# Optimization experiments

Measured on AMD Instinct MI355X. Metric: run time of the kernel, lower is better.

The kernel has to match this reference:

```python
import jax, jax.numpy as jnp
import numpy as np

NUM_HEADS = 6


def dwconv_tokens(tokens, H, W, w, b, stride):
    # tokens: (B, N, C) -> depthwise conv in (B, C, H, W) -> (B, N', C)
    B, N, C = tokens.shape
    x = tokens.transpose(0, 2, 1).reshape(B, C, H, W)
    y = jax.lax.conv_general_dilated(
        x, w, window_strides=(stride, stride), padding=[(1, 1), (1, 1)],
        feature_group_count=C, dimension_numbers=('NCHW', 'OIHW', 'NCHW'))
    y = y + b[None, :, None, None]
    Bc, Cc, Hs, Ws = y.shape
    return y.reshape(Bc, Cc, Hs * Ws).transpose(0, 2, 1), Hs, Ws


def neg_softmax(a):
    # sign(x) * softmax(|x|) along last axis
    return jnp.sign(a) * jax.nn.softmax(jnp.abs(a), axis=-1)


def split_heads(t, nh):
    B, N, C = t.shape
    return t.reshape(B, N, nh, C // nh).transpose(0, 2, 1, 3)  # (B, H, N, d)


def setup_inputs() -> dict:
    key = jax.random.key(0)
    ks = jax.random.split(key, 16)
    B, H, W, C = 8, 56, 56, 384
    N = H * W
    s = 0.02
    inp = {
        'x': jax.random.normal(ks[0], (B, N, C), jnp.float32),
        'H': H, 'W': W,
        'q_w': jax.random.normal(ks[1], (C, C), jnp.float32) * s,
        'q_b': jax.random.normal(ks[2], (C,), jnp.float32) * s,
        'k_w': jax.random.normal(ks[3], (C, C), jnp.float32) * s,
        'k_b': jax.random.normal(ks[4], (C,), jnp.float32) * s,
        'v_w': jax.random.normal(ks[5], (C, C), jnp.float32) * s,
        'v_b': jax.random.normal(ks[6], (C,), jnp.float32) * s,
        'q_dw_w': jax.random.normal(ks[7], (C, 1, 3, 3), jnp.float32) * 0.1,
        'q_dw_b': jax.random.normal(ks[8], (C,), jnp.float32) * s,
        'k_dw_w': jax.random.normal(ks[9], (C, 1, 3, 3), jnp.float32) * 0.1,
        'k_dw_b': jax.random.normal(ks[10], (C,), jnp.float32) * s,
        'v_dw_w': jax.random.normal(ks[11], (C, 1, 3, 3), jnp.float32) * 0.1,
        'v_dw_b': jax.random.normal(ks[12], (C,), jnp.float32) * s,
        'proj_w': jax.random.normal(ks[13], (C, C), jnp.float32) * s,
        'proj_b': jax.random.normal(ks[14], (C,), jnp.float32) * s,
    }
    return inp


def reference(x, H, W, q_w, q_b, k_w, k_b, v_w, v_b,
              q_dw_w, q_dw_b, k_dw_w, k_dw_b, v_dw_w, v_dw_b,
              proj_w, proj_b):
    B, N, C = x.shape
    nh = NUM_HEADS
    hd = C // nh
    scale = hd ** -0.5
    # linear q/k/v (torch Linear: x @ W.T + b)
    q = x @ q_w.T + q_b
    k = x @ k_w.T + k_b
    v = x @ v_w.T + v_b
    # depthwise conv projections (q: stride 1, k/v: stride 2)
    q, Hq, Wq = dwconv_tokens(q, H, W, q_dw_w, q_dw_b, 1)
    k, _, _ = dwconv_tokens(k, H, W, k_dw_w, k_dw_b, 2)
    v, _, _ = dwconv_tokens(v, H, W, v_dw_w, v_dw_b, 2)
    q = split_heads(q, nh)  # (B, nh, Nq, hd)
    k = split_heads(k, nh)  # (B, nh, Nk, hd)
    v = split_heads(v, nh)
    attn = jnp.einsum('bhqd,bhkd->bhqk', q, k) * scale
    attn = neg_softmax(attn)
    out = jnp.einsum('bhqk,bhkd->bhqd', attn, v)
    out = out.transpose(0, 2, 1, 3).reshape(B, -1, C)
    out = out @ proj_w.T + proj_b
    return out
```

## Files before the change

kernel.cpp:

```cpp
#include <hip/hip_runtime.h>
#include <hip/hip_bf16.h>
#include <stdint.h>

typedef __attribute__((ext_vector_type(4))) float f32x4;
typedef __attribute__((ext_vector_type(8))) short s16x8;
typedef __attribute__((ext_vector_type(4))) short s16x4;
typedef __attribute__((ext_vector_type(8))) unsigned short u16x8;

#define NB 8
#define HH 56
#define WW0 56
#define NC 384
#define NQTOK (HH*WW0)
#define NKTOK 784
#define NHEAD 6
#define HDIM 64
#define QSCALE 0.18033688f

__device__ __forceinline__ float bf2f(unsigned short u) {
    union { unsigned int i; float f; } x; x.i = ((unsigned int)u) << 16; return x.f;
}
__device__ __forceinline__ unsigned short f2bf(float f) {
    union { float f; unsigned int i; } x; x.f = f;
    unsigned int r = x.i + 0x7FFFu + ((x.i >> 16) & 1u);
    return (unsigned short)(r >> 16);
}
__device__ __forceinline__ unsigned short f2bf_rn(float f) {
    union { float f; unsigned int i; } x; x.f = f;
    return (unsigned short)((x.i + 0x8000u) >> 16);
}

__global__ __launch_bounds__(256) void prep_all(
    const float* __restrict__ x,
    const float* __restrict__ qw, const float* __restrict__ kw,
    const float* __restrict__ vw, const float* __restrict__ pw,
    const float* __restrict__ qb, const float* __restrict__ kb,
    const float* __restrict__ vb, const float* __restrict__ pb,
    const float* __restrict__ qdw, const float* __restrict__ kdw, const float* __restrict__ vdw,
    unsigned short* __restrict__ xbf, unsigned short* __restrict__ wbf,
    float* __restrict__ wtab, float* __restrict__ ball)
{
    const int bid = blockIdx.x;
    const int t = threadIdx.x;
    if (bid < 4704) {
        int i = bid*256 + t;
        f32x4 a0 = *(const f32x4*)&x[(size_t)i*8];
        f32x4 a1 = *(const f32x4*)&x[(size_t)i*8 + 4];
        u16x8 p;
        #pragma unroll
        for (int j = 0; j < 4; ++j) { p[j] = f2bf(a0[j]); p[j+4] = f2bf(a1[j]); }
        *(u16x8*)&xbf[(size_t)i*8] = p;
    } else if (bid < 4992) {
        int i = (bid - 4704)*256 + t;
        int m = i / 18432;
        const float* s = (m==0) ? qw : ((m==1) ? kw : ((m==2) ? vw : pw));
        int r = i - m*18432;
        f32x4 a0 = *(const f32x4*)&s[(size_t)r*8];
        f32x4 a1 = *(const f32x4*)&s[(size_t)r*8 + 4];
        u16x8 p;
        #pragma unroll
        for (int j = 0; j < 4; ++j) { p[j] = f2bf(a0[j]); p[j+4] = f2bf(a1[j]); }
        *(u16x8*)&wbf[(size_t)i*8] = p;
    } else {
        int j = (bid - 4992)*256 + t;
        if (j < 3*9*NC) {
            int m = j / (9*NC); int r = j - m*(9*NC);
            int tap = r / NC; int c = r - tap*NC;
            const float* src = (m==0) ? qdw : ((m==1) ? kdw : vdw);
            wtab[j] = src[c*9 + tap];
        } else {
            int jj = j - 3*9*NC;
            if (jj < 4*NC) {
                int m = jj / NC, r = jj - m*NC;
                ball[jj] = ((m==0) ? qb : ((m==1) ? kb : ((m==2) ? vb : pb)))[r];
            }
        }
    }
}

template<bool OUT_F32>
__global__ __launch_bounds__(512) void gemm_bt_bf(
    const unsigned short* __restrict__ A,
    const unsigned short* __restrict__ Wall,
    const float* __restrict__ Ball,
    unsigned short* __restrict__ Oa, unsigned short* __restrict__ Ob, unsigned short* __restrict__ Oc,
    float* __restrict__ Of,
    int ntiles)
{
    __shared__ unsigned short lA[256*64];
    __shared__ unsigned short lW[128*64];
    char* lAb = (char*)lA;
    char* lWb = (char*)lW;
    const int bid = blockIdx.x;
    const int nt = bid % ntiles;
    const int mt = bid / ntiles;
    const int mat = nt / 3;
    const int ncol = nt - mat*3;
    const unsigned short* W = Wall + (size_t)mat*NC*NC;
    const float* Bsel = Ball + mat*NC;
    unsigned short* Osel = (mat==0) ? Oa : ((mat==1) ? Ob : Oc);
    const int Mbase = mt*256, Nbase = ncol*128;
    const int t = threadIdx.x;
    const int w = t >> 6, l = t & 63;
    const int wr = w >> 1, wc = w & 1;
    const int lr = l & 15, lg = l >> 4;
    const int swg = (lr & 7) << 4;

    f32x4 acc[4][4] = {};
    for (int kt = 0; kt < 6; ++kt) {
        __syncthreads();
        #pragma unroll
        for (int i = 0; i < 4; ++i) {
            int c = i*512 + t;
            int row = c >> 3, c8 = c & 7;
            int sdst = row*128 + ((c8*16) ^ ((row & 7) << 4));
            *(u16x8*)(lAb + sdst) = *(const u16x8*)&A[(size_t)(Mbase+row)*NC + kt*64 + c8*8];
        }
        #pragma unroll
        for (int i = 0; i < 2; ++i) {
            int c = i*512 + t;
            int row = c >> 3, c8 = c & 7;
            int sdst = row*128 + ((c8*16) ^ ((row & 7) << 4));
            *(u16x8*)(lWb + sdst) = *(const u16x8*)&W[(size_t)(Nbase+row)*NC + kt*64 + c8*8];
        }
        __syncthreads();
        #pragma unroll
        for (int kk = 0; kk < 2; ++kk) {
            s16x8 af[4], bfr[4];
            #pragma unroll
            for (int m = 0; m < 4; ++m)
                af[m] = *(const s16x8*)(lAb + (wr*64 + m*16 + lr)*128 + ((kk*64 + lg*16) ^ swg));
            #pragma unroll
            for (int n = 0; n < 4; ++n)
                bfr[n] = *(const s16x8*)(lWb + (wc*64 + n*16 + lr)*128 + ((kk*64 + lg*16) ^ swg));
            #pragma unroll
            for (int m = 0; m < 4; ++m)
                #pragma unroll
                for (int n = 0; n < 4; ++n)
                    acc[m][n] = __builtin_amdgcn_mfma_f32_16x16x32_bf16(af[m], bfr[n], acc[m][n], 0, 0, 0);
        }
    }
    #pragma unroll
    for (int n = 0; n < 4; ++n) {
        int col = Nbase + wc*64 + n*16 + lr;
        float bias = Bsel[col];
        #pragma unroll
        for (int m = 0; m < 4; ++m) {
            int row0 = Mbase + wr*64 + m*16 + lg*4;
            #pragma unroll
            for (int r = 0; r < 4; ++r) {
                float vv = acc[m][n][r] + bias;
                if (OUT_F32) Of[(size_t)(row0 + r)*NC + col] = vv;
                else Osel[(size_t)(row0 + r)*NC + col] = f2bf(vv);
            }
        }
    }
}

template<int S, int HO, int WO, bool SCALE, int MODE>
__device__ __forceinline__ void dwconv_body(
    int idx,
    const unsigned short* __restrict__ in,
    const float* __restrict__ wt9,
    const float* __restrict__ bias,
    unsigned short* __restrict__ outp)
{
    const int nc8 = NC/8;
    int c8 = idx % nc8; int rest = idx / nc8;
    int wo = rest % WO; rest /= WO;
    int ho = rest % HO; int b = rest / HO;
    int c0 = c8*8;
    f32x4 b0 = *(const f32x4*)&bias[c0];
    f32x4 b1 = *(const f32x4*)&bias[c0+4];
    float acc[8];
    #pragma unroll
    for (int j = 0; j < 4; ++j) { acc[j] = b0[j]; acc[j+4] = b1[j]; }
    #pragma unroll
    for (int kh = 0; kh < 3; ++kh) {
        int h = ho*S + kh - 1;
        if (h < 0 || h >= HH) continue;
        #pragma unroll
        for (int kw = 0; kw < 3; ++kw) {
            int ww = wo*S + kw - 1;
            if (ww < 0 || ww >= WW0) continue;
            int tap = kh*3 + kw;
            u16x8 xv = *(const u16x8*)&in[((size_t)b*(HH*WW0) + h*WW0 + ww)*NC + c0];
            f32x4 w0 = *(const f32x4*)&wt9[tap*NC + c0];
            f32x4 w1 = *(const f32x4*)&wt9[tap*NC + c0 + 4];
            #pragma unroll
            for (int j = 0; j < 4; ++j) {
                acc[j]   += bf2f(xv[j])   * w0[j];
                acc[j+4] += bf2f(xv[j+4]) * w1[j];
            }
        }
    }
    if (SCALE) {
        #pragma unroll
        for (int j = 0; j < 8; ++j) acc[j] *= QSCALE;
    }
    int tok = ho*WO + wo;
    int hh = c0 >> 6, d0 = c0 & 63;
    if (MODE == 0) {
        u16x8 ov;
        #pragma unroll
        for (int j = 0; j < 8; ++j) ov[j] = f2bf(acc[j]);
        *(u16x8*)&outp[((size_t)b*(HO*WO) + tok)*NC + c0] = ov;
    } else if (MODE == 1) {
        u16x8 ov;
        #pragma unroll
        for (int j = 0; j < 8; ++j) ov[j] = f2bf(acc[j]);
        *(u16x8*)&outp[((size_t)(b*NHEAD + hh)*(HO*WO) + tok)*HDIM + d0] = ov;
    } else {
        size_t base = ((size_t)(b*NHEAD + hh)*HDIM + d0)*(HO*WO) + tok;
        #pragma unroll
        for (int j = 0; j < 8; ++j)
            outp[base + (size_t)j*(HO*WO)] = f2bf(acc[j]);
    }
}

__global__ __launch_bounds__(256) void dwconv_kv(
    const unsigned short* __restrict__ preK, const unsigned short* __restrict__ preV,
    const float* __restrict__ wtK, const float* __restrict__ wtV,
    const float* __restrict__ biasK, const float* __restrict__ biasV,
    unsigned short* __restrict__ Kpk, unsigned short* __restrict__ Vt)
{
    const int bid = blockIdx.x;
    if (bid < 1176) {
        int idx = bid*256 + threadIdx.x;
        dwconv_body<2,28,28,false,1>(idx, preK, wtK, biasK, Kpk);
    } else {
        int idx = (bid-1176)*256 + threadIdx.x;
        dwconv_body<2,28,28,false,2>(idx, preV, wtV, biasV, Vt);
    }
}

__global__ __launch_bounds__(256) void dwconv_q(
    const unsigned short* __restrict__ in,
    const float* __restrict__ wt9, const float* __restrict__ bias,
    unsigned short* __restrict__ outp)
{
    int idx = blockIdx.x*256 + threadIdx.x;
    dwconv_body<1,56,56,true,0>(idx, in, wt9, bias, outp);
}

__global__ __launch_bounds__(256) void attn_fwd(
    const unsigned short* __restrict__ Q,
    const unsigned short* __restrict__ Kpk,
    const unsigned short* __restrict__ Vt,
    unsigned short* __restrict__ ctx)
{
    __shared__ unsigned short lK[2][4096];
    __shared__ unsigned short lV[2][4096];
    const int bid = blockIdx.x;
    const int xcd = bid & 7, slot = bid >> 3;
    const int bh = xcd*6 + slot/25;
    const int qt = slot % 25;
    const int b = bh / NHEAD, h = bh - b*NHEAD;
    const int t = threadIdx.x;
    const int w = t >> 6, l = t & 63;
    const int lq = l & 15, lg = l >> 4;
    const int wq0 = qt*128 + w*32;
    const int wq0c = (wq0 > NQTOK-32) ? (NQTOK-32) : wq0;

    const unsigned short* Qb = Q + ((size_t)b*NQTOK + wq0c + lq)*NC + h*HDIM;
    s16x8 qA[2][2];
    qA[0][0] = *(const s16x8*)&Qb[lg*8];
    qA[0][1] = *(const s16x8*)&Qb[32 + lg*8];
    qA[1][0] = *(const s16x8*)&Qb[16*NC + lg*8];
    qA[1][1] = *(const s16x8*)&Qb[16*NC + 32 + lg*8];

    const char* Kg = (const char*)(Kpk + (size_t)bh*NKTOK*HDIM);
    const char* Vg = (const char*)(Vt + (size_t)bh*HDIM*NKTOK);
    char* lKb = (char*)lK;
    char* lVb = (char*)lV;

    const int cr0 = t >> 3;
    const int cr1 = cr0 + 32;
    const int cc  = (t & 7) * 16;
    const int dst0 = cr0*128 + (cc ^ ((cr0 & 7) << 4));
    const int dst1 = cr1*128 + (cc ^ ((cr1 & 7) << 4));

    uint4 rk0, rk1, rv0, rv1;
    #define LOADT(kb) do { \
        rk0 = *(const uint4*)(Kg + (size_t)((kb) + cr0)*128 + cc); \
        rk1 = *(const uint4*)(Kg + (size_t)((kb) + cr1)*128 + cc); \
        rv0 = *(const uint4*)(Vg + (size_t)cr0*1568 + (kb)*2 + cc); \
        rv1 = *(const uint4*)(Vg + (size_t)cr1*1568 + (kb)*2 + cc); \
    } while(0)
    #define WRITET(buf) do { \
        *(uint4*)(lKb + (buf)*8192 + dst0) = rk0; \
        *(uint4*)(lKb + (buf)*8192 + dst1) = rk1; \
        *(uint4*)(lVb + (buf)*8192 + dst0) = rv0; \
        *(uint4*)(lVb + (buf)*8192 + dst1) = rv1; \
    } while(0)

    const int swc = (lq & 7) << 4;
    const int ck0 = (lg*16) ^ swc;
    const int ck1 = (64 + lg*16) ^ swc;

    float ls[2] = {0.f, 0.f};
    f32x4 oacc[2][4] = {};

    LOADT(0);
    WRITET(0);
    LOADT(64);
    __syncthreads();

    for (int kt = 0; kt < 12; ++kt) {
        const int cur = kt & 1;
        if (kt < 11) {
            WRITET(cur ^ 1);
            if (kt < 10) LOADT((kt+2)*64);
        }
        const char* Kl = lKb + cur*8192;
        const char* Vl = lVb + cur*8192;
        f32x4 st[2][4] = {};
        __builtin_amdgcn_s_setprio(1);
        #pragma unroll
        for (int kfr = 0; kfr < 4; ++kfr) {
            int rb = (kfr*16 + lq)*128;
            s16x8 kf0 = *(const s16x8*)(Kl + rb + ck0);
            s16x8 kf1 = *(const s16x8*)(Kl + rb + ck1);
            st[0][kfr] = __builtin_amdgcn_mfma_f32_16x16x32_bf16(kf0, qA[0][0], st[0][kfr], 0,0,0);
            st[0][kfr] = __builtin_amdgcn_mfma_f32_16x16x32_bf16(kf1, qA[0][1], st[0][kfr], 0,0,0);
            st[1][kfr] = __builtin_amdgcn_mfma_f32_16x16x32_bf16(kf0, qA[1][0], st[1][kfr], 0,0,0);
            st[1][kfr] = __builtin_amdgcn_mfma_f32_16x16x32_bf16(kf1, qA[1][1], st[1][kfr], 0,0,0);
        }
        __builtin_amdgcn_s_setprio(0);
        s16x4 pbv[2][4];
        #pragma unroll
        for (int qf = 0; qf < 2; ++qf) {
            float rs = 0.f;
            #pragma unroll
            for (int kfr = 0; kfr < 4; ++kfr)
                #pragma unroll
                for (int r = 0; r < 4; ++r) {
                    float s = st[qf][kfr][r];
                    float e = __builtin_amdgcn_exp2f(fabsf(s));
                    rs += e;
                    pbv[qf][kfr][r] = (short)f2bf_rn(copysignf(e, s));
                }
            ls[qf] += rs;
        }
        __builtin_amdgcn_s_setprio(1);
        #pragma unroll
        for (int ks = 0; ks < 4; ++ks)
            #pragma unroll
            for (int f = 0; f < 4; ++f) {
                int va = (f*16 + lq)*128 + ((ks*32 + lg*8) ^ swc);
                s16x4 vvf = *(const s16x4*)(Vl + va);
                oacc[0][f] = __builtin_amdgcn_mfma_f32_16x16x16bf16_1k(vvf, pbv[0][ks], oacc[0][f], 0,0,0);
                oacc[1][f] = __builtin_amdgcn_mfma_f32_16x16x16bf16_1k(vvf, pbv[1][ks], oacc[1][f], 0,0,0);
            }
        __builtin_amdgcn_s_setprio(0);
        if (kt < 11) __syncthreads();
    }
    {
        const unsigned short* Kb2 = (const unsigned short*)Kg;
        const unsigned short* Vb2 = (const unsigned short*)Vg;
        const unsigned short* kr = &Kb2[(size_t)(768 + lq)*HDIM];
        s16x8 kf0 = *(const s16x8*)&kr[lg*8];
        s16x8 kf1 = *(const s16x8*)&kr[32 + lg*8];
        f32x4 st[2] = {};
        st[0] = __builtin_amdgcn_mfma_f32_16x16x32_bf16(kf0, qA[0][0], st[0], 0,0,0);
        st[0] = __builtin_amdgcn_mfma_f32_16x16x32_bf16(kf1, qA[0][1], st[0], 0,0,0);
        st[1] = __builtin_amdgcn_mfma_f32_16x16x32_bf16(kf0, qA[1][0], st[1], 0,0,0);
        st[1] = __builtin_amdgcn_mfma_f32_16x16x32_bf16(kf1, qA[1][1], st[1], 0,0,0);
        s16x4 vv[4];
        #pragma unroll
        for (int f = 0; f < 4; ++f)
            vv[f] = *(const s16x4*)&Vb2[(size_t)(f*16 + lq)*NKTOK + 768 + lg*4];
        s16x4 pbv[2];
        #pragma unroll
        for (int qf = 0; qf < 2; ++qf) {
            float rs = 0.f;
            #pragma unroll
            for (int r = 0; r < 4; ++r) {
                float s = st[qf][r];
                float e = __builtin_amdgcn_exp2f(fabsf(s));
                rs += e;
                pbv[qf][r] = (short)f2bf_rn(copysignf(e, s));
            }
            ls[qf] += rs;
        }
        #pragma unroll
        for (int f = 0; f < 4; ++f) {
            oacc[0][f] = __builtin_amdgcn_mfma_f32_16x16x16bf16_1k(vv[f], pbv[0], oacc[0][f], 0,0,0);
            oacc[1][f] = __builtin_amdgcn_mfma_f32_16x16x16bf16_1k(vv[f], pbv[1], oacc[1][f], 0,0,0);
        }
    }
    if (wq0 < NQTOK) {
        #pragma unroll
        for (int qf = 0; qf < 2; ++qf) {
            float lr2 = ls[qf];
            lr2 += __shfl_xor(lr2, 16);
            lr2 += __shfl_xor(lr2, 32);
            float inv = 1.f / lr2;
            unsigned short* cb = ctx + ((size_t)b*NQTOK + wq0 + qf*16 + lq)*NC + h*HDIM;
            #pragma unroll
            for (int f = 0; f < 4; ++f) {
                s16x4 o;
                #pragma unroll
                for (int r = 0; r < 4; ++r) o[r] = (short)f2bf(oacc[qf][f][r] * inv);
                *(s16x4*)&cb[f*16 + lg*4] = o;
            }
        }
    }
    #undef LOADT
    #undef WRITET
}

extern "C" void kernel_launch(void* const* d_in, const int* in_sizes, int n_in,
                              void* d_out, int out_size, void* d_ws, size_t ws_size,
                              hipStream_t stream)
{
    (void)in_sizes; (void)n_in; (void)out_size; (void)ws_size;
    const float* x      = (const float*)d_in[0];
    const float* q_w    = (const float*)d_in[3];
    const float* q_b    = (const float*)d_in[4];
    const float* k_w    = (const float*)d_in[5];
    const float* k_b    = (const float*)d_in[6];
    const float* v_w    = (const float*)d_in[7];
    const float* v_b    = (const float*)d_in[8];
    const float* q_dw_w = (const float*)d_in[9];
    const float* q_dw_b = (const float*)d_in[10];
    const float* k_dw_w = (const float*)d_in[11];
    const float* k_dw_b = (const float*)d_in[12];
    const float* v_dw_w = (const float*)d_in[13];
    const float* v_dw_b = (const float*)d_in[14];
    const float* proj_w = (const float*)d_in[15];
    const float* proj_b = (const float*)d_in[16];
    float* outf = (float*)d_out;
    unsigned short* ws  = (unsigned short*)d_ws;

    const size_t nQ  = (size_t)NB*NQTOK*NC;
    const size_t nKc = (size_t)NB*NKTOK*NC;
    unsigned short* preQ = ws;
    unsigned short* preK = ws + nQ;
    unsigned short* Kpk  = ws + 2*nQ;
    unsigned short* Vt   = Kpk + nKc;
    unsigned short* wbf  = Vt + nKc;
    float* wtab = (float*)(wbf + (size_t)4*NC*NC);
    float* ball = wtab + 3*9*NC;
    unsigned short* preV = (unsigned short*)d_out;
    unsigned short* Qc   = (unsigned short*)d_out;
    unsigned short* xbf  = ((unsigned short*)d_out) + nQ;
    unsigned short* ctx  = preK;

    prep_all<<<dim3(5039), dim3(256), 0, stream>>>(
        x, q_w, k_w, v_w, proj_w, q_b, k_b, v_b, proj_b,
        q_dw_w, k_dw_w, v_dw_w, xbf, wbf, wtab, ball);
    gemm_bt_bf<false><<<dim3(98*9), dim3(512), 0, stream>>>(
        xbf, wbf, ball, preQ, preK, preV, nullptr, 9);
    dwconv_kv<<<dim3(2352), dim3(256), 0, stream>>>(
        preK, preV, wtab + 1*9*NC, wtab + 2*9*NC, k_dw_b, v_dw_b, Kpk, Vt);
    dwconv_q<<<dim3(4704), dim3(256), 0, stream>>>(preQ, wtab + 0*9*NC, q_dw_b, Qc);
    attn_fwd<<<dim3(1200), dim3(256), 0, stream>>>(Qc, Kpk, Vt, ctx);
    gemm_bt_bf<true><<<dim3(98*3), dim3(512), 0, stream>>>(
        ctx, wbf + (size_t)3*NC*NC, ball + 3*NC, nullptr, nullptr, nullptr, outf, 3);
}
```

Measured before the change: 180.8 us.

## Merge Q/K/V depthwise convs into one launch and halve attention query tile

Folds the K/V and Q depthwise-conv kernels into a single launch of 7056 blocks. Because the Q conv now runs alongside the V conv, the Q output buffer moves off d_out, where preV lives, and into the xbf region. The attention kernel now gives each wave 16 query rows instead of 32 and each block 64 queries, so 2352 blocks run instead of 1200 and the tail clamp is no longer needed. This removes one launch and raises parallelism for attention. The cost is that each K/V tile loaded into LDS now serves half as many queries, doubling K/V traffic from LDS and global memory per query.

```diff
diff --git a/kernel.cpp b/kernel.cpp
--- a/kernel.cpp
+++ b/kernel.cpp
@@ -218,29 +218,25 @@
     }
 }
 
-__global__ __launch_bounds__(256) void dwconv_kv(
+__global__ __launch_bounds__(256) void dwconv_all(
     const unsigned short* __restrict__ preK, const unsigned short* __restrict__ preV,
-    const float* __restrict__ wtK, const float* __restrict__ wtV,
-    const float* __restrict__ biasK, const float* __restrict__ biasV,
-    unsigned short* __restrict__ Kpk, unsigned short* __restrict__ Vt)
+    const unsigned short* __restrict__ preQ,
+    const float* __restrict__ wtK, const float* __restrict__ wtV, const float* __restrict__ wtQ,
+    const float* __restrict__ biasK, const float* __restrict__ biasV, const float* __restrict__ biasQ,
+    unsigned short* __restrict__ Kpk, unsigned short* __restrict__ Vt,
+    unsigned short* __restrict__ Qc)
 {
     const int bid = blockIdx.x;
     if (bid < 1176) {
         int idx = bid*256 + threadIdx.x;
         dwconv_body<2,28,28,false,1>(idx, preK, wtK, biasK, Kpk);
-    } else {
+    } else if (bid < 2352) {
         int idx = (bid-1176)*256 + threadIdx.x;
         dwconv_body<2,28,28,false,2>(idx, preV, wtV, biasV, Vt);
-    }
-}
-
-__global__ __launch_bounds__(256) void dwconv_q(
-    const unsigned short* __restrict__ in,
-    const float* __restrict__ wt9, const float* __restrict__ bias,
-    unsigned short* __restrict__ outp)
-{
-    int idx = blockIdx.x*256 + threadIdx.x;
-    dwconv_body<1,56,56,true,0>(idx, in, wt9, bias, outp);
+    } else {
+        int idx = (bid-2352)*256 + threadIdx.x;
+        dwconv_body<1,56,56,true,0>(idx, preQ, wtQ, biasQ, Qc);
+    }
 }
 
 __global__ __launch_bounds__(256) void attn_fwd(
@@ -253,21 +249,17 @@
     __shared__ unsigned short lV[2][4096];
     const int bid = blockIdx.x;
     const int xcd = bid & 7, slot = bid >> 3;
-    const int bh = xcd*6 + slot/25;
-    const int qt = slot % 25;
+    const int bh = xcd*6 + slot/49;
+    const int qt = slot % 49;
     const int b = bh / NHEAD, h = bh - b*NHEAD;
     const int t = threadIdx.x;
     const int w = t >> 6, l = t & 63;
     const int lq = l & 15, lg = l >> 4;
-    const int wq0 = qt*128 + w*32;
-    const int wq0c = (wq0 > NQTOK-32) ? (NQTOK-32) : wq0;
-
-    const unsigned short* Qb = Q + ((size_t)b*NQTOK + wq0c + lq)*NC + h*HDIM;
-    s16x8 qA[2][2];
-    qA[0][0] = *(const s16x8*)&Qb[lg*8];
-    qA[0][1] = *(const s16x8*)&Qb[32 + lg*8];
-    qA[1][0] = *(const s16x8*)&Qb[16*NC + lg*8];
-    qA[1][1] = *(const s16x8*)&Qb[16*NC + 32 + lg*8];
+    const int wq0 = qt*64 + w*16;
+
+    const unsigned short* Qb = Q + ((size_t)b*NQTOK + wq0 + lq)*NC + h*HDIM;
+    s16x8 qA0 = *(const s16x8*)&Qb[lg*8];
+    s16x8 qA1 = *(const s16x8*)&Qb[32 + lg*8];
 
     const char* Kg = (const char*)(Kpk + (size_t)bh*NKTOK*HDIM);
     const char* Vg = (const char*)(Vt + (size_t)bh*HDIM*NKTOK);
@@ -298,8 +290,8 @@
     const int ck0 = (lg*16) ^ swc;
     const int ck1 = (64 + lg*16) ^ swc;
 
-    float ls[2] = {0.f, 0.f};
-    f32x4 oacc[2][4] = {};
+    float ls = 0.f;
+    f32x4 oacc[4] = {};
 
     LOADT(0);
     WRITET(0);
@@ -314,33 +306,30 @@
         }
         const char* Kl = lKb + cur*8192;
         const char* Vl = lVb + cur*8192;
-        f32x4 st[2][4] = {};
+        f32x4 st[4] = {};
         __builtin_amdgcn_s_setprio(1);
         #pragma unroll
         for (int kfr = 0; kfr < 4; ++kfr) {
             int rb = (kfr*16 + lq)*128;
             s16x8 kf0 = *(const s16x8*)(Kl + rb + ck0);
             s16x8 kf1 = *(const s16x8*)(Kl + rb + ck1);
-            st[0][kfr] = __builtin_amdgcn_mfma_f32_16x16x32_bf16(kf0, qA[0][0], st[0][kfr], 0,0,0);
-            st[0][kfr] = __builtin_amdgcn_mfma_f32_16x16x32_bf16(kf1, qA[0][1], st[0][kfr], 0,0,0);
-            st[1][kfr] = __builtin_amdgcn_mfma_f32_16x16x32_bf16(kf0, qA[1][0], st[1][kfr], 0,0,0);
-            st[1][kfr] = __builtin_amdgcn_mfma_f32_16x16x32_bf16(kf1, qA[1][1], st[1][kfr], 0,0,0);
+            st[kfr] = __builtin_amdgcn_mfma_f32_16x16x32_bf16(kf0, qA0, st[kfr], 0,0,0);
+            st[kfr] = __builtin_amdgcn_mfma_f32_16x16x32_bf16(kf1, qA1, st[kfr], 0,0,0);
         }
         __builtin_amdgcn_s_setprio(0);
-        s16x4 pbv[2][4];
-        #pragma unroll
-        for (int qf = 0; qf < 2; ++qf) {
+        s16x4 pbv[4];
+        {
             float rs = 0.f;
             #pragma unroll
             for (int kfr = 0; kfr < 4; ++kfr)
                 #pragma unroll
                 for (int r = 0; r < 4; ++r) {
-                    float s = st[qf][kfr][r];
+                    float s = st[kfr][r];
                     float e = __builtin_amdgcn_exp2f(fabsf(s));
                     rs += e;
-                    pbv[qf][kfr][r] = (short)f2bf_rn(copysignf(e, s));
+                    pbv[kfr][r] = (short)f2bf_rn(copysignf(e, s));
                 }
-            ls[qf] += rs;
+            ls += rs;
         }
         __builtin_amdgcn_s_setprio(1);
         #pragma unroll
@@ -349,8 +338,7 @@
             for (int f = 0; f < 4; ++f) {
                 int va = (f*16 + lq)*128 + ((ks*32 + lg*8) ^ swc);
                 s16x4 vvf = *(const s16x4*)(Vl + va);
-                oacc[0][f] = __builtin_amdgcn_mfma_f32_16x16x16bf16_1k(vvf, pbv[0][ks], oacc[0][f], 0,0,0);
-                oacc[1][f] = __builtin_amdgcn_mfma_f32_16x16x16bf16_1k(vvf, pbv[1][ks], oacc[1][f], 0,0,0);
+                oacc[f] = __builtin_amdgcn_mfma_f32_16x16x16bf16_1k(vvf, pbv[ks], oacc[f], 0,0,0);
             }
         __builtin_amdgcn_s_setprio(0);
         if (kt < 11) __syncthreads();
@@ -361,49 +349,39 @@
         const unsigned short* kr = &Kb2[(size_t)(768 + lq)*HDIM];
         s16x8 kf0 = *(const s16x8*)&kr[lg*8];
         s16x8 kf1 = *(const s16x8*)&kr[32 + lg*8];
-        f32x4 st[2] = {};
-        st[0] = __builtin_amdgcn_mfma_f32_16x16x32_bf16(kf0, qA[0][0], st[0], 0,0,0);
-        st[0] = __builtin_amdgcn_mfma_f32_16x16x32_bf16(kf1, qA[0][1], st[0], 0,0,0);
-        st[1] = __builtin_amdgcn_mfma_f32_16x16x32_bf16(kf0, qA[1][0], st[1], 0,0,0);
-        st[1] = __builtin_amdgcn_mfma_f32_16x16x32_bf16(kf1, qA[1][1], st[1], 0,0,0);
+        f32x4 st = {};
+        st = __builtin_amdgcn_mfma_f32_16x16x32_bf16(kf0, qA0, st, 0,0,0);
+        st = __builtin_amdgcn_mfma_f32_16x16x32_bf16(kf1, qA1, st, 0,0,0);
         s16x4 vv[4];
         #pragma unroll
         for (int f = 0; f < 4; ++f)
             vv[f] = *(const s16x4*)&Vb2[(size_t)(f*16 + lq)*NKTOK + 768 + lg*4];
-        s16x4 pbv[2];
-        #pragma unroll
-        for (int qf = 0; qf < 2; ++qf) {
-            float rs = 0.f;
-            #pragma unroll
-            for (int r = 0; r < 4; ++r) {
-                float s = st[qf][r];
-                float e = __builtin_amdgcn_exp2f(fabsf(s));
-                rs += e;
-                pbv[qf][r] = (short)f2bf_rn(copysignf(e, s));
-            }
-            ls[qf] += rs;
-        }
+        s16x4 pbv;
+        float rs = 0.f;
+        #pragma unroll
+        for (int r = 0; r < 4; ++r) {
+            float s = st[r];
+            float e = __builtin_amdgcn_exp2f(fabsf(s));
+            rs += e;
+            pbv[r] = (short)f2bf_rn(copysignf(e, s));
+        }
+        ls += rs;
+        #pragma unroll
+        for (int f = 0; f < 4; ++f)
+            oacc[f] = __builtin_amdgcn_mfma_f32_16x16x16bf16_1k(vv[f], pbv, oacc[f], 0,0,0);
+    }
+    {
+        float lr2 = ls;
+        lr2 += __shfl_xor(lr2, 16);
+        lr2 += __shfl_xor(lr2, 32);
+        float inv = 1.f / lr2;
+        unsigned short* cb = ctx + ((size_t)b*NQTOK + wq0 + lq)*NC + h*HDIM;
         #pragma unroll
         for (int f = 0; f < 4; ++f) {
-            oacc[0][f] = __builtin_amdgcn_mfma_f32_16x16x16bf16_1k(vv[f], pbv[0], oacc[0][f], 0,0,0);
-            oacc[1][f] = __builtin_amdgcn_mfma_f32_16x16x16bf16_1k(vv[f], pbv[1], oacc[1][f], 0,0,0);
-        }
-    }
-    if (wq0 < NQTOK) {
-        #pragma unroll
-        for (int qf = 0; qf < 2; ++qf) {
-            float lr2 = ls[qf];
-            lr2 += __shfl_xor(lr2, 16);
-            lr2 += __shfl_xor(lr2, 32);
-            float inv = 1.f / lr2;
-            unsigned short* cb = ctx + ((size_t)b*NQTOK + wq0 + qf*16 + lq)*NC + h*HDIM;
-            #pragma unroll
-            for (int f = 0; f < 4; ++f) {
-                s16x4 o;
-                #pragma unroll
-                for (int r = 0; r < 4; ++r) o[r] = (short)f2bf(oacc[qf][f][r] * inv);
-                *(s16x4*)&cb[f*16 + lg*4] = o;
-            }
+            s16x4 o;
+            #pragma unroll
+            for (int r = 0; r < 4; ++r) o[r] = (short)f2bf(oacc[f][r] * inv);
+            *(s16x4*)&cb[f*16 + lg*4] = o;
         }
     }
     #undef LOADT
@@ -443,8 +421,8 @@
     float* wtab = (float*)(wbf + (size_t)4*NC*NC);
     float* ball = wtab + 3*9*NC;
     unsigned short* preV = (unsigned short*)d_out;
-    unsigned short* Qc   = (unsigned short*)d_out;
     unsigned short* xbf  = ((unsigned short*)d_out) + nQ;
+    unsigned short* Qc   = xbf;
     unsigned short* ctx  = preK;
 
     prep_all<<<dim3(5039), dim3(256), 0, stream>>>(
@@ -452,10 +430,11 @@
         q_dw_w, k_dw_w, v_dw_w, xbf, wbf, wtab, ball);
     gemm_bt_bf<false><<<dim3(98*9), dim3(512), 0, stream>>>(
         xbf, wbf, ball, preQ, preK, preV, nullptr, 9);
-    dwconv_kv<<<dim3(2352), dim3(256), 0, stream>>>(
-        preK, preV, wtab + 1*9*NC, wtab + 2*9*NC, k_dw_b, v_dw_b, Kpk, Vt);
-    dwconv_q<<<dim3(4704), dim3(256), 0, stream>>>(preQ, wtab + 0*9*NC, q_dw_b, Qc);
-    attn_fwd<<<dim3(1200), dim3(256), 0, stream>>>(Qc, Kpk, Vt, ctx);
+    dwconv_all<<<dim3(7056), dim3(256), 0, stream>>>(
+        preK, preV, preQ,
+        wtab + 1*9*NC, wtab + 2*9*NC, wtab + 0*9*NC,
+        k_dw_b, v_dw_b, q_dw_b, Kpk, Vt, Qc);
+    attn_fwd<<<dim3(2352), dim3(256), 0, stream>>>(Qc, Kpk, Vt, ctx);
     gemm_bt_bf<true><<<dim3(98*3), dim3(512), 0, stream>>>(
         ctx, wbf + (size_t)3*NC*NC, ball + 3*NC, nullptr, nullptr, nullptr, outf, 3);
 }
```

Measured after the change: 173.0 us. 4.3% less time.
